# Performance work log

Hardware: AMD Instinct MI355X
Metric: run time of the kernel (lower is better)

Reference implementation:

```python
import jax, jax.numpy as jnp
import numpy as np

B, T, D = 2, 2048, 1024
H, Dh = 16, 64


def setup_inputs() -> dict:
    key = jax.random.key(0)
    ks = jax.random.split(key, 5)
    s = 0.02
    return {
        "x": jax.random.normal(ks[0], (B, T, D), dtype=jnp.float32),
        "attention_mask": jnp.ones((B, T), dtype=jnp.int32),
        "Wq": jax.random.normal(ks[1], (D, H * Dh), dtype=jnp.float32) * s,
        "Wk": jax.random.normal(ks[2], (D, H * Dh), dtype=jnp.float32) * s,
        "Wv": jax.random.normal(ks[3], (D, H * Dh), dtype=jnp.float32) * s,
        "Wo": jax.random.normal(ks[4], (H * Dh, D), dtype=jnp.float32) * s,
    }


def reference(x, attention_mask, Wq, Wk, Wv, Wo):
    scale = Dh ** -0.5
    # projections: [B,T,H,Dh]
    q = (x @ Wq).reshape(B, T, H, Dh)
    k = (x @ Wk).reshape(B, T, H, Dh)
    v = (x @ Wv).reshape(B, T, H, Dh)
    # scores: [B,H,T,T]
    attn = jnp.einsum("bqhd,bkhd->bhqk", q, k) * scale
    mask = attention_mask.astype(jnp.float32)[:, None, None, :]  # [B,1,1,T]
    attn = attn + (1.0 - mask) * -1e9
    attn = jax.nn.softmax(attn, axis=-1)
    # dropout p=0.0 (eval) -> identity
    out = jnp.einsum("bhqk,bkhd->bqhd", attn, v).reshape(B, T, H * Dh)
    return out @ Wo
```

## Files before the change

kernel.cpp:

```cpp
#include <hip/hip_runtime.h>
#include <stdint.h>

typedef unsigned short u16;
typedef unsigned int u32;

constexpr int CB = 2, CT = 2048, CH = 16, CDH = 64, CD = 1024;

typedef __attribute__((ext_vector_type(8))) short bf16x8;
typedef __attribute__((ext_vector_type(4))) float f32x4;
typedef __attribute__((ext_vector_type(16))) float f32x16;

typedef __attribute__((address_space(1))) const u32 as1_cu32;
typedef __attribute__((address_space(3))) u32 as3_u32;

__device__ __forceinline__ void gload_lds16(const void* g, void* l) {
  __builtin_amdgcn_global_load_lds((as1_cu32*)g, (as3_u32*)l, 16, 0, 0);
}

__device__ __forceinline__ u16 f2b(float f) {
  u32 x = __float_as_uint(f);
  u32 r = (x + 0x7fffu + ((x >> 16) & 1u)) >> 16;
  return (u16)r;
}

#if __has_builtin(__builtin_amdgcn_cvt_pk_bf16_f32)
typedef __attribute__((ext_vector_type(2))) __bf16 v2bf;
__device__ __forceinline__ u32 pk2(float a, float b) {
  v2bf r = __builtin_amdgcn_cvt_pk_bf16_f32(a, b);
  union { v2bf v; u32 u; } cv; cv.v = r; return cv.u;
}
#else
__device__ __forceinline__ u32 pk2(float a, float b) {
  return (u32)f2b(a) | ((u32)f2b(b) << 16);
}
#endif

__device__ __forceinline__ float b2f(u32 lo16) { return __uint_as_float(lo16 << 16); }

__device__ __forceinline__ void store_out(u16* p, float v) { *p = f2b(v); }
__device__ __forceinline__ void store_out(float* p, float v) { *p = v; }

__device__ __forceinline__ void plswap(u32& a, u32& b, int hf) {
  u32 ta = (u32)__shfl_xor((int)a, 32, 64);
  u32 tb = (u32)__shfl_xor((int)b, 32, 64);
  u32 na = hf ? tb : a;
  u32 nb = hf ? b : ta;
  a = na; b = nb;
}

__global__ __launch_bounds__(256) void prep_k(const float* __restrict__ x,
                                              const float* __restrict__ Wq,
                                              const float* __restrict__ Wk,
                                              const float* __restrict__ Wv,
                                              const float* __restrict__ Wo,
                                              u16* __restrict__ Xb,
                                              u16* __restrict__ Wt) {
  __shared__ float tile[32][33];
  int bid = blockIdx.x, t = threadIdx.x;
  if (bid < 4096) {
    int i = bid * 256 + t;
    float4 v = ((const float4*)x)[i];
    ushort4 r;
    r.x = f2b(v.x); r.y = f2b(v.y); r.z = f2b(v.z); r.w = f2b(v.w);
    ((ushort4*)Xb)[i] = r;
  } else {
    int tid2 = bid - 4096;
    int mat = tid2 >> 10, b2 = tid2 & 1023;
    const float* W = (mat == 0) ? Wq : (mat == 1) ? Wk : (mat == 2) ? Wv : Wo;
    u16* dst = Wt + (size_t)mat * 1048576;
    int bx = (b2 & 31) * 32, by = (b2 >> 5) * 32;
    int tx = t & 31, ty = t >> 5;
    #pragma unroll
    for (int i = ty; i < 32; i += 8) tile[i][tx] = W[(size_t)(by + i) * CD + bx + tx];
    __syncthreads();
    #pragma unroll
    for (int i = ty; i < 32; i += 8)
      dst[(size_t)(bx + i) * CD + by + tx] = f2b(tile[tx][i]);
  }
}

template <typename OT>
__global__ __launch_bounds__(256) void gemm_bt_k(const u16* __restrict__ A,
                                                 const u16* __restrict__ Bt,
                                                 OT* __restrict__ Cout,
                                                 int K, size_t subStride) {
  __shared__ __align__(16) u16 As[128 * 32];
  __shared__ __align__(16) u16 Bs[128 * 32];
  int t = threadIdx.x;
  int lane = t & 63, w = t >> 6;
  int m = lane & 15, quad = lane >> 4;
  int wrow = w >> 1, wcol = w & 1;
  int m0 = blockIdx.y * 128, n0 = blockIdx.x * 128;

  f32x4 acc[4][4];
  #pragma unroll
  for (int i = 0; i < 4; i++)
    #pragma unroll
    for (int j = 0; j < 4; j++) acc[i][j] = (f32x4){0.f, 0.f, 0.f, 0.f};

  for (int k0 = 0; k0 < K; k0 += 32) {
    __syncthreads();
    #pragma unroll
    for (int p = 0; p < 2; p++) {
      int idx = p * 256 + t;
      int row = idx >> 2, c = idx & 3;
      int cc = c ^ (row & 3);
      gload_lds16(A + (size_t)(m0 + row) * K + k0 + cc * 8,
                  As + (size_t)(p * 256 + (t & 192)) * 8);
      gload_lds16(Bt + (size_t)(n0 + row) * K + k0 + cc * 8,
                  Bs + (size_t)(p * 256 + (t & 192)) * 8);
    }
    __syncthreads();
    bf16x8 af[4], bfr[4];
    #pragma unroll
    for (int mt = 0; mt < 4; mt++) {
      int r = wrow * 64 + mt * 16 + m;
      af[mt] = *(const bf16x8*)&As[r * 32 + ((quad ^ (r & 3)) * 8)];
    }
    #pragma unroll
    for (int nt = 0; nt < 4; nt++) {
      int r = wcol * 64 + nt * 16 + m;
      bfr[nt] = *(const bf16x8*)&Bs[r * 32 + ((quad ^ (r & 3)) * 8)];
    }
    #pragma unroll
    for (int mt = 0; mt < 4; mt++)
      #pragma unroll
      for (int nt = 0; nt < 4; nt++)
        acc[mt][nt] = __builtin_amdgcn_mfma_f32_16x16x32_bf16(af[mt], bfr[nt],
                                                              acc[mt][nt], 0, 0, 0);
  }

  #pragma unroll
  for (int mt = 0; mt < 4; mt++) {
    #pragma unroll
    for (int nt = 0; nt < 4; nt++) {
      int c = n0 + wcol * 64 + nt * 16 + m;
      OT* outp = Cout + (size_t)(c >> 10) * subStride + (c & 1023);
      #pragma unroll
      for (int rr = 0; rr < 4; rr++) {
        int r = m0 + wrow * 64 + mt * 16 + quad * 4 + rr;
        store_out(outp + (size_t)r * CD, acc[mt][nt][rr]);
      }
    }
  }
}

__global__ __launch_bounds__(256, 4) void attn_k(const u16* __restrict__ Qb,
                                                 const u16* __restrict__ Kb,
                                                 const u16* __restrict__ Vb,
                                                 const int* __restrict__ mask,
                                                 u16* __restrict__ Opart,
                                                 float* __restrict__ Lpart) {
  __shared__ __align__(16) u16 Ks[64 * 64];
  __shared__ __align__(16) u32 VsD[64 * 36];

  int t = threadIdx.x, lane = t & 63, w = t >> 6;
  int c32 = lane & 31, hf = lane >> 5;
  int qt = blockIdx.x, head = blockIdx.y;
  int b = blockIdx.z & 1, half = blockIdx.z >> 1;
  int kv0 = half * 1024;
  int gid = (b * 16 + head) * 16 + qt;

  const u16* Qg = Qb + ((size_t)(b * CT + qt * 128 + w * 32 + c32)) * CD + head * CDH;
  bf16x8 qbf[4];
  #pragma unroll
  for (int kc = 0; kc < 4; kc++)
    qbf[kc] = *(const bf16x8*)(Qg + kc * 16 + hf * 8);

  const int* mk = mask + b * CT + kv0;
  int localAny = 0;
  for (int i = t; i < 1024; i += 256) localAny |= (mk[i] == 0);
  int anyM = __syncthreads_or(localAny);

  f32x16 oacc[2];
  #pragma unroll
  for (int dt = 0; dt < 2; dt++)
    #pragma unroll
    for (int r = 0; r < 16; r++) oacc[dt][r] = 0.f;
  float lp = 0.f;

  const u16* Kg0 = Kb + ((size_t)(b * CT + kv0)) * CD + head * CDH;
  const u16* Vg0 = Vb + ((size_t)(b * CT + kv0)) * CD + head * CDH;

  int vpr = t >> 3, vdg = t & 7;
  const u16* VgT = Vg0 + (size_t)(2 * vpr) * CD + vdg * 8;
  uint4 va = *(const uint4*)VgT;
  uint4 vb2 = *(const uint4*)(VgT + CD);

  for (int kv = 0; kv < 1024; kv += 64) {
    __syncthreads();
    #pragma unroll
    for (int p = 0; p < 2; p++) {
      int idx = p * 256 + t;
      int row = idx >> 3, cc = (idx & 7) ^ (row & 7);
      gload_lds16(Kg0 + (size_t)(kv + row) * CD + cc * 8,
                  Ks + (size_t)(p * 256 + (t & 192)) * 8);
    }
    {
      const u32* pa = (const u32*)&va;
      const u32* pb = (const u32*)&vb2;
      u32* dst = VsD + (size_t)vdg * 288 + (vpr ^ (vdg << 2));
      #pragma unroll
      for (int j = 0; j < 8; j++) {
        u32 lo_dw = pa[j >> 1], hi_dw = pb[j >> 1];
        u32 pk = (j & 1) ? __builtin_amdgcn_perm(hi_dw, lo_dw, 0x07060302u)
                         : __builtin_amdgcn_perm(hi_dw, lo_dw, 0x05040100u);
        dst[j * 36] = pk;
      }
    }
    __syncthreads();
    if (kv + 64 < 1024) {
      VgT = Vg0 + (size_t)(kv + 64 + 2 * vpr) * CD + vdg * 8;
      va = *(const uint4*)VgT;
      vb2 = *(const uint4*)(VgT + CD);
    }

    #pragma unroll
    for (int kt = 0; kt < 2; kt++) {
      f32x16 sv;
      #pragma unroll
      for (int r = 0; r < 16; r++) sv[r] = 0.f;
      int key = kt * 32 + c32;
      #pragma unroll
      for (int kc = 0; kc < 4; kc++) {
        int ch = kc * 2 + hf;
        bf16x8 af = *(const bf16x8*)&Ks[key * 64 + ((ch ^ (key & 7)) * 8)];
        sv = __builtin_amdgcn_mfma_f32_32x32x16_bf16(af, qbf[kc], sv, 0, 0, 0);
      }
      float pv[16];
      #pragma unroll
      for (int r = 0; r < 16; r++) {
        float xs = sv[r] * 0.125f;
        if (anyM) {
          int mi = kv + kt * 32 + (r & 3) + 8 * (r >> 2) + 4 * hf;
          xs += mk[mi] ? 0.f : -1.0e9f;
        }
        pv[r] = __expf(fminf(xs, 30.f));
        lp += pv[r];
      }
      u32 pk[8];
      #pragma unroll
      for (int i = 0; i < 8; i++) pk[i] = pk2(pv[2 * i], pv[2 * i + 1]);
      #pragma unroll
      for (int c = 0; c < 2; c++) {
        u32 d0 = pk[4 * c + 0], d2 = pk[4 * c + 2];
        u32 d1 = pk[4 * c + 1], d3 = pk[4 * c + 3];
        plswap(d0, d2, hf);
        plswap(d1, d3, hf);
        union { u32 u[4]; bf16x8 v; } pf;
        pf.u[0] = d0; pf.u[1] = d1; pf.u[2] = d2; pf.u[3] = d3;
        int prb = kt * 16 + c * 8 + hf * 4;
        #pragma unroll
        for (int dt = 0; dt < 2; dt++) {
          int d = dt * 32 + c32;
          const u32* vp = VsD + d * 36 + (prb ^ ((d >> 3) << 2));
          bf16x8 vf = *(const bf16x8*)vp;
          oacc[dt] = __builtin_amdgcn_mfma_f32_32x32x16_bf16(vf, pf.v, oacc[dt], 0, 0, 0);
        }
      }
    }
  }

  float lT = lp + __shfl_xor(lp, 32, 64);
  float linv = 1.f / lT;
  u16* Op = Opart + ((size_t)(half * 512 + gid) * 128 + w * 32 + c32) * 64;
  #pragma unroll
  for (int dt = 0; dt < 2; dt++) {
    #pragma unroll
    for (int g = 0; g < 4; g++) {
      float o0 = oacc[dt][4 * g + 0] * linv, o1 = oacc[dt][4 * g + 1] * linv;
      float o2 = oacc[dt][4 * g + 2] * linv, o3 = oacc[dt][4 * g + 3] * linv;
      uint2 pw;
      pw.x = pk2(o0, o1);
      pw.y = pk2(o2, o3);
      *(uint2*)(Op + dt * 32 + 8 * g + 4 * hf) = pw;
    }
  }
  if (lane < 32) Lpart[(size_t)(half * 512 + gid) * 128 + w * 32 + lane] = lT;
}

__global__ __launch_bounds__(256) void combine_k(const u16* __restrict__ Opart,
                                                 const float* __restrict__ Lpart,
                                                 u16* __restrict__ Ob) {
  int fid = blockIdx.x * 256 + threadIdx.x;
  int gid = fid >> 11;
  int rem = fid & 2047;
  int r = rem >> 4, d = (rem & 15) * 4;
  int b = gid >> 8, head = (gid >> 4) & 15, qt = gid & 15;
  size_t i0 = ((size_t)gid * 128 + r) * 64 + d;
  size_t i1 = ((size_t)(512 + gid) * 128 + r) * 64 + d;
  uint2 A = *(const uint2*)(Opart + i0);
  uint2 Bv = *(const uint2*)(Opart + i1);
  float la = Lpart[gid * 128 + r], lb = Lpart[(512 + gid) * 128 + r];
  float inv = 1.f / (la + lb);
  float wa = la * inv, wb = lb * inv;
  float o0 = wa * b2f(A.x & 0xffffu) + wb * b2f(Bv.x & 0xffffu);
  float o1 = wa * b2f(A.x >> 16) + wb * b2f(Bv.x >> 16);
  float o2 = wa * b2f(A.y & 0xffffu) + wb * b2f(Bv.y & 0xffffu);
  float o3 = wa * b2f(A.y >> 16) + wb * b2f(Bv.y >> 16);
  uint2 pw;
  pw.x = pk2(o0, o1);
  pw.y = pk2(o2, o3);
  size_t trow = (size_t)b * CT + qt * 128 + r;
  *(uint2*)(Ob + trow * CD + head * CDH + d) = pw;
}

extern "C" void kernel_launch(void* const* d_in, const int* in_sizes, int n_in,
                              void* d_out, int out_size, void* d_ws, size_t ws_size,
                              hipStream_t stream) {
  const float* x  = (const float*)d_in[0];
  const int* mask = (const int*)d_in[1];
  const float* Wq = (const float*)d_in[2];
  const float* Wk = (const float*)d_in[3];
  const float* Wv = (const float*)d_in[4];
  const float* Wo = (const float*)d_in[5];
  float* out = (float*)d_out;

  u16* Xb    = (u16*)d_ws;
  u16* Wqkv  = Xb + (size_t)4096 * 1024;
  u16* WoT   = Wqkv + (size_t)3072 * 1024;
  u16* Qb    = Wqkv + (size_t)4096 * 1024;
  u16* Ob    = Qb + (size_t)3 * 4096 * 1024;
  u16* Opart = Ob + (size_t)4096 * 1024;
  float* Lpart = (float*)(Opart + (size_t)2 * 512 * 128 * 64);

  prep_k<<<8192, 256, 0, stream>>>(x, Wq, Wk, Wv, Wo, Xb, Wqkv);
  gemm_bt_k<u16><<<dim3(24, 32), 256, 0, stream>>>(Xb, Wqkv, Qb, 1024,
                                                   (size_t)4096 * 1024);
  attn_k<<<dim3(16, 16, 4), 256, 0, stream>>>(Qb, Qb + (size_t)4096 * 1024,
                                              Qb + (size_t)2 * 4096 * 1024, mask,
                                              Opart, Lpart);
  combine_k<<<4096, 256, 0, stream>>>(Opart, Lpart, Ob);
  gemm_bt_k<float><<<dim3(8, 32), 256, 0, stream>>>(Ob, WoT, out, 1024, 0);
}
```

Baseline: 220.3 us.

## Process two query groups per wave in attention, add 64-wide output GEMM, permlane swap

The attention kernel now runs 128 threads, with each wave handling 64 query rows (two 32-row groups). Each K fragment read from LDS is reused for two score MFMAs and each V fragment for two PV MFMAs, which halves LDS traffic per FLOP. The output projection switches to a new 128x64-tile GEMM that launches twice as many blocks, for better CU coverage on a 1024-wide output. The half-wave swap uses the permlane32_swap builtin when it is available. In exchange, the attention kernel carries more register pressure and has fewer threads per block to share the loading work.

```diff
diff --git a/kernel.cpp b/kernel.cpp
--- a/kernel.cpp
+++ b/kernel.cpp
@@ -40,6 +40,12 @@
 __device__ __forceinline__ void store_out(u16* p, float v) { *p = f2b(v); }
 __device__ __forceinline__ void store_out(float* p, float v) { *p = v; }
 
+#if __has_builtin(__builtin_amdgcn_permlane32_swap)
+__device__ __forceinline__ void plswap(u32& a, u32& b, int) {
+  auto r = __builtin_amdgcn_permlane32_swap(a, b, false, false);
+  a = (u32)r[0]; b = (u32)r[1];
+}
+#else
 __device__ __forceinline__ void plswap(u32& a, u32& b, int hf) {
   u32 ta = (u32)__shfl_xor((int)a, 32, 64);
   u32 tb = (u32)__shfl_xor((int)b, 32, 64);
@@ -47,6 +53,7 @@
   u32 nb = hf ? b : ta;
   a = na; b = nb;
 }
+#endif
 
 __global__ __launch_bounds__(256) void prep_k(const float* __restrict__ x,
                                               const float* __restrict__ Wq,
@@ -145,7 +152,72 @@
   }
 }
 
-__global__ __launch_bounds__(256, 4) void attn_k(const u16* __restrict__ Qb,
+__global__ __launch_bounds__(256) void gemm_bt64_k(const u16* __restrict__ A,
+                                                   const u16* __restrict__ Bt,
+                                                   float* __restrict__ Cout, int K) {
+  __shared__ __align__(16) u16 As[128 * 32];
+  __shared__ __align__(16) u16 Bs[64 * 32];
+  int t = threadIdx.x;
+  int lane = t & 63, w = t >> 6;
+  int m = lane & 15, quad = lane >> 4;
+  int wrow = w >> 1, wcol = w & 1;
+  int m0 = blockIdx.y * 128, n0 = blockIdx.x * 64;
+
+  f32x4 acc[4][2];
+  #pragma unroll
+  for (int i = 0; i < 4; i++)
+    #pragma unroll
+    for (int j = 0; j < 2; j++) acc[i][j] = (f32x4){0.f, 0.f, 0.f, 0.f};
+
+  for (int k0 = 0; k0 < K; k0 += 32) {
+    __syncthreads();
+    #pragma unroll
+    for (int p = 0; p < 2; p++) {
+      int idx = p * 256 + t;
+      int row = idx >> 2, cc = (idx & 3) ^ (row & 3);
+      gload_lds16(A + (size_t)(m0 + row) * K + k0 + cc * 8,
+                  As + (size_t)(p * 256 + (t & 192)) * 8);
+    }
+    {
+      int row = t >> 2, cc = (t & 3) ^ (row & 3);
+      gload_lds16(Bt + (size_t)(n0 + row) * K + k0 + cc * 8,
+                  Bs + (size_t)(t & 192) * 8);
+    }
+    __syncthreads();
+    bf16x8 af[4], bfr[2];
+    #pragma unroll
+    for (int mt = 0; mt < 4; mt++) {
+      int r = wrow * 64 + mt * 16 + m;
+      af[mt] = *(const bf16x8*)&As[r * 32 + ((quad ^ (r & 3)) * 8)];
+    }
+    #pragma unroll
+    for (int nt = 0; nt < 2; nt++) {
+      int r = wcol * 32 + nt * 16 + m;
+      bfr[nt] = *(const bf16x8*)&Bs[r * 32 + ((quad ^ (r & 3)) * 8)];
+    }
+    #pragma unroll
+    for (int mt = 0; mt < 4; mt++)
+      #pragma unroll
+      for (int nt = 0; nt < 2; nt++)
+        acc[mt][nt] = __builtin_amdgcn_mfma_f32_16x16x32_bf16(af[mt], bfr[nt],
+                                                              acc[mt][nt], 0, 0, 0);
+  }
+
+  #pragma unroll
+  for (int mt = 0; mt < 4; mt++) {
+    #pragma unroll
+    for (int nt = 0; nt < 2; nt++) {
+      int c = n0 + wcol * 32 + nt * 16 + m;
+      #pragma unroll
+      for (int rr = 0; rr < 4; rr++) {
+        int r = m0 + wrow * 64 + mt * 16 + quad * 4 + rr;
+        Cout[(size_t)r * CD + c] = acc[mt][nt][rr];
+      }
+    }
+  }
+}
+
+__global__ __launch_bounds__(128, 2) void attn_k(const u16* __restrict__ Qb,
                                                  const u16* __restrict__ Kb,
                                                  const u16* __restrict__ Vb,
                                                  const int* __restrict__ mask,
@@ -161,122 +233,158 @@
   int kv0 = half * 1024;
   int gid = (b * 16 + head) * 16 + qt;
 
-  const u16* Qg = Qb + ((size_t)(b * CT + qt * 128 + w * 32 + c32)) * CD + head * CDH;
-  bf16x8 qbf[4];
-  #pragma unroll
-  for (int kc = 0; kc < 4; kc++)
-    qbf[kc] = *(const bf16x8*)(Qg + kc * 16 + hf * 8);
+  bf16x8 qbf[2][4];
+  #pragma unroll
+  for (int qg = 0; qg < 2; qg++) {
+    const u16* Qg = Qb + ((size_t)(b * CT + qt * 128 + w * 64 + qg * 32 + c32)) * CD + head * CDH;
+    #pragma unroll
+    for (int kc = 0; kc < 4; kc++)
+      qbf[qg][kc] = *(const bf16x8*)(Qg + kc * 16 + hf * 8);
+  }
 
   const int* mk = mask + b * CT + kv0;
   int localAny = 0;
-  for (int i = t; i < 1024; i += 256) localAny |= (mk[i] == 0);
+  for (int i = t; i < 1024; i += 128) localAny |= (mk[i] == 0);
   int anyM = __syncthreads_or(localAny);
 
-  f32x16 oacc[2];
-  #pragma unroll
-  for (int dt = 0; dt < 2; dt++)
-    #pragma unroll
-    for (int r = 0; r < 16; r++) oacc[dt][r] = 0.f;
-  float lp = 0.f;
+  f32x16 oacc[2][2];
+  #pragma unroll
+  for (int qg = 0; qg < 2; qg++)
+    #pragma unroll
+    for (int dt = 0; dt < 2; dt++)
+      #pragma unroll
+      for (int r = 0; r < 16; r++) oacc[qg][dt][r] = 0.f;
+  float lp[2] = {0.f, 0.f};
 
   const u16* Kg0 = Kb + ((size_t)(b * CT + kv0)) * CD + head * CDH;
   const u16* Vg0 = Vb + ((size_t)(b * CT + kv0)) * CD + head * CDH;
 
-  int vpr = t >> 3, vdg = t & 7;
-  const u16* VgT = Vg0 + (size_t)(2 * vpr) * CD + vdg * 8;
-  uint4 va = *(const uint4*)VgT;
-  uint4 vb2 = *(const uint4*)(VgT + CD);
+  int vpr[2], vdg[2];
+  uint4 va[2], vb2[2];
+  #pragma unroll
+  for (int rep = 0; rep < 2; rep++) {
+    int u = rep * 128 + t;
+    vpr[rep] = u >> 3; vdg[rep] = u & 7;
+    const u16* VgT = Vg0 + (size_t)(2 * vpr[rep]) * CD + vdg[rep] * 8;
+    va[rep] = *(const uint4*)VgT;
+    vb2[rep] = *(const uint4*)(VgT + CD);
+  }
 
   for (int kv = 0; kv < 1024; kv += 64) {
     __syncthreads();
     #pragma unroll
-    for (int p = 0; p < 2; p++) {
-      int idx = p * 256 + t;
+    for (int p = 0; p < 4; p++) {
+      int idx = p * 128 + t;
       int row = idx >> 3, cc = (idx & 7) ^ (row & 7);
       gload_lds16(Kg0 + (size_t)(kv + row) * CD + cc * 8,
-                  Ks + (size_t)(p * 256 + (t & 192)) * 8);
-    }
-    {
-      const u32* pa = (const u32*)&va;
-      const u32* pb = (const u32*)&vb2;
-      u32* dst = VsD + (size_t)vdg * 288 + (vpr ^ (vdg << 2));
+                  Ks + (size_t)(p * 128 + (t & 64)) * 8);
+    }
+    #pragma unroll
+    for (int rep = 0; rep < 2; rep++) {
+      const u32* pa = (const u32*)&va[rep];
+      const u32* pb = (const u32*)&vb2[rep];
+      u32* dst = VsD + (size_t)vdg[rep] * 288 + (vpr[rep] ^ (vdg[rep] << 2));
       #pragma unroll
       for (int j = 0; j < 8; j++) {
         u32 lo_dw = pa[j >> 1], hi_dw = pb[j >> 1];
-        u32 pk = (j & 1) ? __builtin_amdgcn_perm(hi_dw, lo_dw, 0x07060302u)
-                         : __builtin_amdgcn_perm(hi_dw, lo_dw, 0x05040100u);
-        dst[j * 36] = pk;
+        u32 pkv = (j & 1) ? __builtin_amdgcn_perm(hi_dw, lo_dw, 0x07060302u)
+                          : __builtin_amdgcn_perm(hi_dw, lo_dw, 0x05040100u);
+        dst[j * 36] = pkv;
       }
     }
     __syncthreads();
     if (kv + 64 < 1024) {
-      VgT = Vg0 + (size_t)(kv + 64 + 2 * vpr) * CD + vdg * 8;
-      va = *(const uint4*)VgT;
-      vb2 = *(const uint4*)(VgT + CD);
+      #pragma unroll
+      for (int rep = 0; rep < 2; rep++) {
+        const u16* VgT = Vg0 + (size_t)(kv + 64 + 2 * vpr[rep]) * CD + vdg[rep] * 8;
+        va[rep] = *(const uint4*)VgT;
+        vb2[rep] = *(const uint4*)(VgT + CD);
+      }
     }
 
     #pragma unroll
     for (int kt = 0; kt < 2; kt++) {
-      f32x16 sv;
-      #pragma unroll
-      for (int r = 0; r < 16; r++) sv[r] = 0.f;
+      bf16x8 af[4];
       int key = kt * 32 + c32;
       #pragma unroll
       for (int kc = 0; kc < 4; kc++) {
         int ch = kc * 2 + hf;
-        bf16x8 af = *(const bf16x8*)&Ks[key * 64 + ((ch ^ (key & 7)) * 8)];
-        sv = __builtin_amdgcn_mfma_f32_32x32x16_bf16(af, qbf[kc], sv, 0, 0, 0);
-      }
-      float pv[16];
-      #pragma unroll
-      for (int r = 0; r < 16; r++) {
-        float xs = sv[r] * 0.125f;
-        if (anyM) {
-          int mi = kv + kt * 32 + (r & 3) + 8 * (r >> 2) + 4 * hf;
-          xs += mk[mi] ? 0.f : -1.0e9f;
+        af[kc] = *(const bf16x8*)&Ks[key * 64 + ((ch ^ (key & 7)) * 8)];
+      }
+      u32 pfr[2][2][4];
+      #pragma unroll
+      for (int qg = 0; qg < 2; qg++) {
+        f32x16 sv;
+        #pragma unroll
+        for (int r = 0; r < 16; r++) sv[r] = 0.f;
+        #pragma unroll
+        for (int kc = 0; kc < 4; kc++)
+          sv = __builtin_amdgcn_mfma_f32_32x32x16_bf16(af[kc], qbf[qg][kc], sv, 0, 0, 0);
+        u32 pk[8];
+        #pragma unroll
+        for (int i = 0; i < 8; i++) {
+          float x0 = sv[2 * i] * 0.125f, x1 = sv[2 * i + 1] * 0.125f;
+          if (anyM) {
+            int r0 = 2 * i, r1 = 2 * i + 1;
+            int mi0 = kv + kt * 32 + (r0 & 3) + 8 * (r0 >> 2) + 4 * hf;
+            int mi1 = kv + kt * 32 + (r1 & 3) + 8 * (r1 >> 2) + 4 * hf;
+            x0 += mk[mi0] ? 0.f : -1.0e9f;
+            x1 += mk[mi1] ? 0.f : -1.0e9f;
+          }
+          float p0 = __expf(fminf(x0, 30.f));
+          float p1 = __expf(fminf(x1, 30.f));
+          lp[qg] += p0 + p1;
+          pk[i] = pk2(p0, p1);
         }
-        pv[r] = __expf(fminf(xs, 30.f));
-        lp += pv[r];
-      }
-      u32 pk[8];
-      #pragma unroll
-      for (int i = 0; i < 8; i++) pk[i] = pk2(pv[2 * i], pv[2 * i + 1]);
+        #pragma unroll
+        for (int c = 0; c < 2; c++) {
+          u32 d0 = pk[4 * c + 0], d2 = pk[4 * c + 2];
+          u32 d1 = pk[4 * c + 1], d3 = pk[4 * c + 3];
+          plswap(d0, d2, hf);
+          plswap(d1, d3, hf);
+          pfr[qg][c][0] = d0; pfr[qg][c][1] = d1;
+          pfr[qg][c][2] = d2; pfr[qg][c][3] = d3;
+        }
+      }
       #pragma unroll
       for (int c = 0; c < 2; c++) {
-        u32 d0 = pk[4 * c + 0], d2 = pk[4 * c + 2];
-        u32 d1 = pk[4 * c + 1], d3 = pk[4 * c + 3];
-        plswap(d0, d2, hf);
-        plswap(d1, d3, hf);
-        union { u32 u[4]; bf16x8 v; } pf;
-        pf.u[0] = d0; pf.u[1] = d1; pf.u[2] = d2; pf.u[3] = d3;
         int prb = kt * 16 + c * 8 + hf * 4;
         #pragma unroll
         for (int dt = 0; dt < 2; dt++) {
           int d = dt * 32 + c32;
           const u32* vp = VsD + d * 36 + (prb ^ ((d >> 3) << 2));
           bf16x8 vf = *(const bf16x8*)vp;
-          oacc[dt] = __builtin_amdgcn_mfma_f32_32x32x16_bf16(vf, pf.v, oacc[dt], 0, 0, 0);
+          union { u32 u[4]; bf16x8 v; } pf0, pf1;
+          #pragma unroll
+          for (int q2 = 0; q2 < 4; q2++) { pf0.u[q2] = pfr[0][c][q2]; pf1.u[q2] = pfr[1][c][q2]; }
+          oacc[0][dt] = __builtin_amdgcn_mfma_f32_32x32x16_bf16(vf, pf0.v, oacc[0][dt], 0, 0, 0);
+          oacc[1][dt] = __builtin_amdgcn_mfma_f32_32x32x16_bf16(vf, pf1.v, oacc[1][dt], 0, 0, 0);
         }
       }
     }
   }
 
-  float lT = lp + __shfl_xor(lp, 32, 64);
-  float linv = 1.f / lT;
-  u16* Op = Opart + ((size_t)(half * 512 + gid) * 128 + w * 32 + c32) * 64;
-  #pragma unroll
-  for (int dt = 0; dt < 2; dt++) {
-    #pragma unroll
-    for (int g = 0; g < 4; g++) {
-      float o0 = oacc[dt][4 * g + 0] * linv, o1 = oacc[dt][4 * g + 1] * linv;
-      float o2 = oacc[dt][4 * g + 2] * linv, o3 = oacc[dt][4 * g + 3] * linv;
-      uint2 pw;
-      pw.x = pk2(o0, o1);
-      pw.y = pk2(o2, o3);
-      *(uint2*)(Op + dt * 32 + 8 * g + 4 * hf) = pw;
-    }
-  }
-  if (lane < 32) Lpart[(size_t)(half * 512 + gid) * 128 + w * 32 + lane] = lT;
+  #pragma unroll
+  for (int qg = 0; qg < 2; qg++) {
+    float lT = lp[qg] + __shfl_xor(lp[qg], 32, 64);
+    float linv = 1.f / lT;
+    int qrow = w * 64 + qg * 32 + c32;
+    u16* Op = Opart + ((size_t)(half * 512 + gid) * 128 + qrow) * 64;
+    #pragma unroll
+    for (int dt = 0; dt < 2; dt++) {
+      #pragma unroll
+      for (int g = 0; g < 4; g++) {
+        float o0 = oacc[qg][dt][4 * g + 0] * linv, o1 = oacc[qg][dt][4 * g + 1] * linv;
+        float o2 = oacc[qg][dt][4 * g + 2] * linv, o3 = oacc[qg][dt][4 * g + 3] * linv;
+        uint2 pw;
+        pw.x = pk2(o0, o1);
+        pw.y = pk2(o2, o3);
+        *(uint2*)(Op + dt * 32 + 8 * g + 4 * hf) = pw;
+      }
+    }
+    if (hf == 0)
+      Lpart[(size_t)(half * 512 + gid) * 128 + w * 64 + qg * 32 + c32] = lT;
+  }
 }
 
 __global__ __launch_bounds__(256) void combine_k(const u16* __restrict__ Opart,
@@ -327,9 +435,9 @@
   prep_k<<<8192, 256, 0, stream>>>(x, Wq, Wk, Wv, Wo, Xb, Wqkv);
   gemm_bt_k<u16><<<dim3(24, 32), 256, 0, stream>>>(Xb, Wqkv, Qb, 1024,
                                                    (size_t)4096 * 1024);
-  attn_k<<<dim3(16, 16, 4), 256, 0, stream>>>(Qb, Qb + (size_t)4096 * 1024,
+  attn_k<<<dim3(16, 16, 4), 128, 0, stream>>>(Qb, Qb + (size_t)4096 * 1024,
                                               Qb + (size_t)2 * 4096 * 1024, mask,
                                               Opart, Lpart);
   combine_k<<<4096, 256, 0, stream>>>(Opart, Lpart, Ob);
-  gemm_bt_k<float><<<dim3(8, 32), 256, 0, stream>>>(Ob, WoT, out, 1024, 0);
-}
+  gemm_bt64_k<<<dim3(16, 32), 256, 0, stream>>>(Ob, WoT, out, 1024);
+}
```

New measurement: 218.8 us. About the same (-0.7%).
